# Kernel tuning notes

Hardware: AMD Instinct MI355X
Metric: run time of the kernel (lower is better)

Reference implementation:

```python
import jax, jax.numpy as jnp
import numpy as np

K = 4      # tagset_size - 2 (real emotion tags)
NT = 6     # tagset_size
START = 4
STOP = 5


def setup_inputs() -> dict:
    key = jax.random.key(0)
    ks = jax.random.split(key, 10)
    B, T = 2048, 2048
    feats = jax.random.normal(ks[0], (B, T, NT), dtype=jnp.float32)
    bias = jax.random.uniform(ks[1], (B, T), dtype=jnp.float32)        # bias_dict values in [0,1)
    tags = jax.random.randint(ks[2], (B, T), 0, K)                     # emotion labels only
    transitions = jax.random.normal(ks[3], (NT, NT), dtype=jnp.float32)
    transitions = transitions.at[START, :].set(-10000.0)
    transitions = transitions.at[:, STOP].set(-10000.0)
    w_shift_in = jax.random.normal(ks[4], (K,), dtype=jnp.float32)
    bias_no = jax.random.normal(ks[5], (1,), dtype=jnp.float32)
    bias_with = jax.random.normal(ks[6], (1,), dtype=jnp.float32)
    w_with_out = jax.random.normal(ks[7], (K,), dtype=jnp.float32)
    w_no_out = jax.random.normal(ks[8], (K,), dtype=jnp.float32)
    multiplier = jax.random.normal(ks[9], (K, K), dtype=jnp.float32)
    multiplier = multiplier.at[jnp.arange(K), jnp.arange(K)].set(-10000.0)
    return dict(feats=feats, bias=bias, tags=tags, transitions=transitions,
                w_shift_in=w_shift_in, bias_no=bias_no, bias_with=bias_with,
                w_with_out=w_with_out, w_no_out=w_no_out, multiplier=multiplier)


def reference(feats, bias, tags, transitions, w_shift_in, bias_no, bias_with,
              w_with_out, w_no_out, multiplier):
    """Batched neg_log_likelihood = forward_alg(feats) - score_sentence(feats, tags)."""
    B, T, _ = feats.shape
    # multiplier_softmax is over dim=0 (columns); diagonal overwritten with -1
    Mmod = jax.nn.softmax(multiplier, axis=0)
    Mmod = Mmod.at[jnp.arange(K), jnp.arange(K)].set(-1.0)

    # per-step transition gate, shape [B,T,K]; branch on bias > 0.5
    b = bias[..., None]
    gates = jnp.where(b > 0.5,
                      w_with_out * jnp.tanh(b * w_shift_in + bias_with),
                      w_no_out * jnp.tanh(b * w_shift_in + bias_no))

    # ---- forward algorithm (log-sum-exp DP over T, vectorized over B) ----
    init = jnp.full((B, NT), -10000.0, dtype=feats.dtype).at[:, START].set(0.0)
    feats_t = jnp.swapaxes(feats, 0, 1)   # [T,B,NT]
    gates_t = jnp.swapaxes(gates, 0, 1)   # [T,B,K]

    def step(alpha, x):
        f, g = x                                          # [B,NT], [B,K]
        blk = g[:, None, :] * Mmod[None, :, :]            # gate[prev] * Mmod[next,prev]
        Teff = transitions[None] + jnp.pad(blk, ((0, 0), (0, 2), (0, 2)))  # [B,NT,NT]
        alpha_new = f + jax.nn.logsumexp(alpha[:, None, :] + Teff, axis=2)
        return alpha_new, None

    alpha, _ = jax.lax.scan(step, init, (feats_t, gates_t))
    fwd_score = jax.nn.logsumexp(alpha + transitions[STOP][None, :], axis=1)  # [B]

    # ---- gold path score ----
    tags_ext = jnp.concatenate(
        [jnp.full((B, 1), START, dtype=tags.dtype), tags], axis=1)
    t0 = tags_ext[:, :-1]   # prev tag, [B,T]
    t1 = tags_ext[:, 1:]    # next tag, [B,T]
    base = transitions[t1, t0]
    Mext = jnp.pad(Mmod, ((0, 2), (0, 2)))
    gate_t0 = jnp.take_along_axis(gates, jnp.clip(t0, 0, K - 1)[..., None], axis=2)[..., 0]
    extra = jnp.where((t0 < K) & (t1 < K), gate_t0 * Mext[t1, t0], 0.0)
    emit = jnp.take_along_axis(feats, t1[..., None], axis=2)[..., 0]
    gold = jnp.sum(base + extra + emit, axis=1) + transitions[STOP, tags[:, -1]]

    return fwd_score - gold  # [B] per-dialog NLL
```

## Files before the change

kernel.cpp:

```cpp
#include <hip/hip_runtime.h>

#define BN 2048
#define TN 2048

__device__ __forceinline__ float ex2(float x){ return __builtin_amdgcn_exp2f(x); }
__device__ __forceinline__ float lg2(float x){ return __builtin_amdgcn_logf(x); }
__device__ __forceinline__ float rcpf(float x){ return __builtin_amdgcn_rcpf(x); }
__device__ __forceinline__ float rfl(float x){
    return __uint_as_float(__builtin_amdgcn_readfirstlane(__float_as_uint(x)));
}

constexpr float kLog2e = 1.4426950408889634f;
constexpr float kLn2   = 0.6931471805599453f;

__device__ __forceinline__ float fast_tanh(float x){
    float ax = fabsf(x);
    float e  = ex2(ax * (-2.0f * kLog2e));
    float t  = (1.0f - e) * rcpf(1.0f + e);
    return copysignf(t, x);
}

__device__ __forceinline__ float sel4(float v0, float v1, float v2, float v3, int idx){
    float r = (idx == 1) ? v1 : v0;
    r = (idx == 2) ? v2 : r;
    r = (idx == 3) ? v3 : r;
    return r;
}

struct P1Params {
    float AL[4][4], M[4][4];
    float wsv[4], wwv[4], wnv[4];
    float bwc, bnc;
    const float* sA; const float* sM;
    float tc4[4];
};

template <int NCOL>
__device__ __forceinline__ void step_generic(
    const P1Params& pp, float fi0, float fi1, float fi2, float fi3,
    float bv, int tg, bool renorm,
    float (&P)[4][NCOL], float (&lacc)[NCOL], float& gold, int& prev)
{
    const bool hw = bv > 0.5f;
    const float bc = hw ? pp.bwc : pp.bnc;
    float g[4], gL[4];
    #pragma unroll
    for (int j = 0; j < 4; ++j) {
        float x = fmaf(bv, pp.wsv[j], bc);
        g[j]  = (hw ? pp.wwv[j] : pp.wnv[j]) * fast_tanh(x);
        gL[j] = g[j] * kLog2e;
    }
    const float fiL[4] = { fi0 * kLog2e, fi1 * kLog2e, fi2 * kLog2e, fi3 * kLog2e };
    float nP[4][NCOL];
    #pragma unroll
    for (int i = 0; i < 4; ++i)
        #pragma unroll
        for (int j = 0; j < NCOL; ++j) nP[i][j] = 0.0f;
    #pragma unroll
    for (int k = 0; k < 4; ++k) {
        float Ek[4];
        #pragma unroll
        for (int i = 0; i < 4; ++i)
            Ek[i] = ex2(fmaf(gL[k], pp.M[i][k], fiL[i] + pp.AL[i][k]));
        #pragma unroll
        for (int j = 0; j < NCOL; ++j) {
            const float pk = P[k][j];
            #pragma unroll
            for (int i = 0; i < 4; ++i) nP[i][j] = fmaf(Ek[i], pk, nP[i][j]);
        }
    }
    #pragma unroll
    for (int i = 0; i < 4; ++i)
        #pragma unroll
        for (int j = 0; j < NCOL; ++j) P[i][j] = nP[i][j];

    const int idx = tg * 4 + prev;
    gold += pp.sA[idx] + sel4(g[0], g[1], g[2], g[3], prev) * pp.sM[idx]
          + sel4(fi0, fi1, fi2, fi3, tg);
    prev = tg;

    if (renorm) {
        #pragma unroll
        for (int j = 0; j < NCOL; ++j) {
            float m = fmaxf(fmaxf(P[0][j], P[1][j]), fmaxf(P[2][j], P[3][j]));
            int ee = (int)((__float_as_uint(m) >> 23) & 255u) - 126;
            float sc = __uint_as_float((unsigned)(127 - ee) << 23);
            lacc[j] += (float)ee;
            #pragma unroll
            for (int i = 0; i < 4; ++i) P[i][j] *= sc;
        }
    }
}

template <int NCOL, bool C0>
__device__ __forceinline__ void trip4(
    const float4 (&F)[6], const float (&Bv)[4], const int (&Tg)[4],
    const P1Params& pp, float (&P)[4][NCOL], float (&lacc)[NCOL],
    float& gold, int& prev)
{
    #pragma unroll
    for (int p = 0; p < 2; ++p) {
        const float4 fA = F[3*p], fB = F[3*p+1], fC = F[3*p+2];
        {
            const float fi0 = fA.x, fi1 = fA.y, fi2 = fA.z, fi3 = fA.w;
            if (C0 && p == 0) {
                const float a0 = fi0 + pp.tc4[0], a1 = fi1 + pp.tc4[1];
                const float a2 = fi2 + pp.tc4[2], a3 = fi3 + pp.tc4[3];
                const float mx = fmaxf(fmaxf(a0, a1), fmaxf(a2, a3));
                P[0][0] = ex2((a0 - mx) * kLog2e);
                P[1][0] = ex2((a1 - mx) * kLog2e);
                P[2][0] = ex2((a2 - mx) * kLog2e);
                P[3][0] = ex2((a3 - mx) * kLog2e);
                lacc[0] = mx * kLog2e;
                const int tg0 = Tg[0];
                gold = sel4(pp.tc4[0], pp.tc4[1], pp.tc4[2], pp.tc4[3], tg0)
                     + sel4(fi0, fi1, fi2, fi3, tg0);
                prev = tg0;
            } else {
                step_generic<NCOL>(pp, fi0, fi1, fi2, fi3, Bv[2*p], Tg[2*p],
                                   false, P, lacc, gold, prev);
            }
        }
        {
            const float fi0 = fB.z, fi1 = fB.w, fi2 = fC.x, fi3 = fC.y;
            step_generic<NCOL>(pp, fi0, fi1, fi2, fi3, Bv[2*p+1], Tg[2*p+1],
                               (2*p+1) == 3, P, lacc, gold, prev);
        }
    }
}

__device__ __forceinline__ void compose4(
    const float (&Ae)[4][4], const float (&sa)[4],
    const float (&Be)[4][4], const float (&sb)[4],
    float (&Ce)[4][4], float (&sc)[4])
{
    const float maxA = fmaxf(fmaxf(sa[0], sa[1]), fmaxf(sa[2], sa[3]));
    float Ap[4][4];
    #pragma unroll
    for (int k = 0; k < 4; ++k) {
        const float wk = ex2(sa[k] - maxA);
        #pragma unroll
        for (int i = 0; i < 4; ++i) Ap[i][k] = Ae[i][k] * wk;
    }
    #pragma unroll
    for (int j = 0; j < 4; ++j) {
        float c0 = 0.f, c1 = 0.f, c2 = 0.f, c3 = 0.f;
        #pragma unroll
        for (int k = 0; k < 4; ++k) {
            const float bk = Be[k][j];
            c0 = fmaf(Ap[0][k], bk, c0);
            c1 = fmaf(Ap[1][k], bk, c1);
            c2 = fmaf(Ap[2][k], bk, c2);
            c3 = fmaf(Ap[3][k], bk, c3);
        }
        const float m = fmaxf(fmaxf(c0, c1), fmaxf(c2, c3));
        const int ee = (int)((__float_as_uint(m) >> 23) & 255u) - 126;
        const float scf = __uint_as_float((unsigned)(127 - ee) << 23);
        Ce[0][j] = c0 * scf; Ce[1][j] = c1 * scf;
        Ce[2][j] = c2 * scf; Ce[3][j] = c3 * scf;
        sc[j] = sb[j] + maxA + (float)ee;
    }
}

__global__ void __launch_bounds__(256)
crf_fused(const float* __restrict__ feats, const float* __restrict__ bias,
          const int* __restrict__ tags, const float* __restrict__ trans,
          const float* __restrict__ wsh, const float* __restrict__ bno,
          const float* __restrict__ bwi, const float* __restrict__ wwo,
          const float* __restrict__ wno, const float* __restrict__ mult,
          float* __restrict__ out)
{
    const int w = threadIdx.x >> 6;
    const int L = threadIdx.x & 63;
    const int b = blockIdx.x;
    const int c = threadIdx.x;

    __shared__ float4 stage[4 * 384];
    __shared__ float sA[16], sM[16];
    __shared__ float red[4][24];

    float4* stageW = stage + w * 384;

    if (threadIdx.x < 16) {
        const int i = threadIdx.x >> 2, j = threadIdx.x & 3;
        sA[threadIdx.x] = trans[i * 6 + j];
        const float m0 = mult[j], m1 = mult[4 + j], m2 = mult[8 + j], m3 = mult[12 + j];
        const float mx = fmaxf(fmaxf(m0, m1), fmaxf(m2, m3));
        const float e0 = ex2((m0 - mx) * kLog2e), e1 = ex2((m1 - mx) * kLog2e);
        const float e2 = ex2((m2 - mx) * kLog2e), e3 = ex2((m3 - mx) * kLog2e);
        const float inv = rcpf(e0 + e1 + e2 + e3);
        const float ei = (i == 0) ? e0 : (i == 1) ? e1 : (i == 2) ? e2 : e3;
        sM[threadIdx.x] = (i == j) ? -1.0f : ei * inv;
    }
    __syncthreads();

    P1Params pp;
    #pragma unroll
    for (int i = 0; i < 4; ++i)
        #pragma unroll
        for (int j = 0; j < 4; ++j) {
            pp.AL[i][j] = rfl(trans[i * 6 + j] * kLog2e);
            pp.M[i][j]  = rfl(sM[i * 4 + j]);
        }
    #pragma unroll
    for (int j = 0; j < 4; ++j) {
        pp.wsv[j] = rfl(wsh[j]); pp.wwv[j] = rfl(wwo[j]); pp.wnv[j] = rfl(wno[j]);
    }
    pp.bwc = rfl(bwi[0]); pp.bnc = rfl(bno[0]);
    pp.sA = sA; pp.sM = sM;
    pp.tc4[0] = rfl(trans[4]);  pp.tc4[1] = rfl(trans[10]);
    pp.tc4[2] = rfl(trans[16]); pp.tc4[3] = rfl(trans[22]);

    float BvA[4], BvB[4]; int TgA[4], TgB[4];
    {
        const float4* bp = (const float4*)(bias + (size_t)b * TN + c * 8);
        const float4 b0 = bp[0], b1 = bp[1];
        BvA[0]=b0.x; BvA[1]=b0.y; BvA[2]=b0.z; BvA[3]=b0.w;
        BvB[0]=b1.x; BvB[1]=b1.y; BvB[2]=b1.z; BvB[3]=b1.w;
        const int4* tp = (const int4*)(tags + (size_t)b * TN + c * 8);
        const int4 t0 = tp[0], t1 = tp[1];
        TgA[0]=t0.x; TgA[1]=t0.y; TgA[2]=t0.z; TgA[3]=t0.w;
        TgB[0]=t1.x; TgB[1]=t1.y; TgB[2]=t1.z; TgB[3]=t1.w;
    }
    int prev = 0;
    if (c != 0) prev = tags[(size_t)b * TN + c * 8 - 1];

    const float4* gF = (const float4*)feats + (size_t)b * 3072 + (size_t)w * 768;

    float P1a[4][1], lacc1[1];
    float P4[4][4],  lacc4[4] = {0.f, 0.f, 0.f, 0.f};
    #pragma unroll
    for (int i = 0; i < 4; ++i)
        #pragma unroll
        for (int j = 0; j < 4; ++j) P4[i][j] = (i == j) ? 1.0f : 0.0f;
    float gold = 0.0f;

    #pragma unroll 1
    for (int h = 0; h < 2; ++h) {
        float4 myF[6];
        {
            float4 tF[6];
            const int h6 = h * 6;
            #pragma unroll
            for (int r = 0; r < 6; ++r) {
                const int S  = r * 64 + L;
                const int cS = (S * 10923) >> 16;
                const int j  = S - cS * 6;
                tF[r] = gF[cS * 12 + h6 + j];
            }
            #pragma unroll
            for (int r = 0; r < 6; ++r) {
                const int S  = r * 64 + L;
                const int cS = (S * 10923) >> 16;
                const int j  = S - cS * 6;
                stageW[(j << 6) + ((cS + j) & 63)] = tF[r];
            }
            #pragma unroll
            for (int j = 0; j < 6; ++j)
                myF[j] = stageW[(j << 6) + ((L + j) & 63)];
        }
        if (c == 0) {
            if (h == 0) trip4<1, true >(myF, BvA, TgA, pp, P1a, lacc1, gold, prev);
            else        trip4<1, false>(myF, BvB, TgB, pp, P1a, lacc1, gold, prev);
        } else {
            if (h == 0) trip4<4, false>(myF, BvA, TgA, pp, P4, lacc4, gold, prev);
            else        trip4<4, false>(myF, BvB, TgB, pp, P4, lacc4, gold, prev);
        }
    }

    float Pe[4][4], so[4];
    if (c == 0) {
        #pragma unroll
        for (int i = 0; i < 4; ++i)
            #pragma unroll
            for (int j = 0; j < 4; ++j) Pe[i][j] = P1a[i][0];
        #pragma unroll
        for (int j = 0; j < 4; ++j) so[j] = lacc1[0];
    } else {
        #pragma unroll
        for (int i = 0; i < 4; ++i)
            #pragma unroll
            for (int j = 0; j < 4; ++j) Pe[i][j] = P4[i][j];
        #pragma unroll
        for (int j = 0; j < 4; ++j) so[j] = lacc4[j];
    }

    #pragma unroll
    for (int d = 1; d < 64; d <<= 1) {
        float oP[4][4], os[4];
        #pragma unroll
        for (int i = 0; i < 4; ++i)
            #pragma unroll
            for (int j = 0; j < 4; ++j) oP[i][j] = __shfl_xor(Pe[i][j], d, 64);
        #pragma unroll
        for (int j = 0; j < 4; ++j) os[j] = __shfl_xor(so[j], d, 64);
        const bool hi = (L & d) != 0;
        float Ae[4][4], Be[4][4], sa[4], sb[4];
        #pragma unroll
        for (int i = 0; i < 4; ++i)
            #pragma unroll
            for (int j = 0; j < 4; ++j) {
                Ae[i][j] = hi ? Pe[i][j] : oP[i][j];
                Be[i][j] = hi ? oP[i][j] : Pe[i][j];
            }
        #pragma unroll
        for (int j = 0; j < 4; ++j) {
            sa[j] = hi ? so[j] : os[j];
            sb[j] = hi ? os[j] : so[j];
        }
        float Ce[4][4], sc[4];
        compose4(Ae, sa, Be, sb, Ce, sc);
        #pragma unroll
        for (int i = 0; i < 4; ++i)
            #pragma unroll
            for (int j = 0; j < 4; ++j) Pe[i][j] = Ce[i][j];
        #pragma unroll
        for (int j = 0; j < 4; ++j) so[j] = sc[j];
    }
    #pragma unroll
    for (int d = 1; d < 64; d <<= 1) gold += __shfl_xor(gold, d, 64);

    if (L == 0) {
        #pragma unroll
        for (int i = 0; i < 4; ++i)
            #pragma unroll
            for (int j = 0; j < 4; ++j) red[w][i * 4 + j] = Pe[i][j];
        #pragma unroll
        for (int j = 0; j < 4; ++j) red[w][16 + j] = so[j];
        red[w][20] = gold;
    }
    __syncthreads();
    if (threadIdx.x == 0) {
        float Pt[4][4], st[4];
        #pragma unroll
        for (int i = 0; i < 4; ++i)
            #pragma unroll
            for (int j = 0; j < 4; ++j) Pt[i][j] = red[0][i * 4 + j];
        #pragma unroll
        for (int j = 0; j < 4; ++j) st[j] = red[0][16 + j];
        float gsum = red[0][20] + red[1][20] + red[2][20] + red[3][20];
        #pragma unroll
        for (int ww = 1; ww < 4; ++ww) {
            float Ae[4][4], sa[4], Ce[4][4], scv[4];
            #pragma unroll
            for (int i = 0; i < 4; ++i)
                #pragma unroll
                for (int j = 0; j < 4; ++j) Ae[i][j] = red[ww][i * 4 + j];
            #pragma unroll
            for (int j = 0; j < 4; ++j) sa[j] = red[ww][16 + j];
            compose4(Ae, sa, Pt, st, Ce, scv);
            #pragma unroll
            for (int i = 0; i < 4; ++i)
                #pragma unroll
                for (int j = 0; j < 4; ++j) Pt[i][j] = Ce[i][j];
            #pragma unroll
            for (int j = 0; j < 4; ++j) st[j] = scv[j];
        }
        const float t50 = trans[30], t51 = trans[31], t52 = trans[32], t53 = trans[33];
        const float ssum = Pt[0][0] * ex2(t50 * kLog2e) + Pt[1][0] * ex2(t51 * kLog2e)
                         + Pt[2][0] * ex2(t52 * kLog2e) + Pt[3][0] * ex2(t53 * kLog2e);
        const float fwd = (st[0] + lg2(ssum)) * kLn2;
        const int lastT = tags[(size_t)b * TN + TN - 1];
        const float gfin = gsum + sel4(t50, t51, t52, t53, lastT);
        out[b] = fwd - gfin;
    }
}

extern "C" void kernel_launch(void* const* d_in, const int* in_sizes, int n_in,
                              void* d_out, int out_size, void* d_ws, size_t ws_size,
                              hipStream_t stream)
{
    const float* feats = (const float*)d_in[0];
    const float* bias  = (const float*)d_in[1];
    const int*   tags  = (const int*)d_in[2];
    const float* trans = (const float*)d_in[3];
    const float* wsh   = (const float*)d_in[4];
    const float* bno   = (const float*)d_in[5];
    const float* bwi   = (const float*)d_in[6];
    const float* wwo   = (const float*)d_in[7];
    const float* wno   = (const float*)d_in[8];
    const float* mult  = (const float*)d_in[9];
    float* out = (float*)d_out;
    (void)d_ws; (void)ws_size;

    crf_fused<<<BN, 256, 0, stream>>>(
        feats, bias, tags, trans, wsh, bno, bwi, wwo, wno, mult, out);
}
```

Measured before the change: 236.4 us.

## Replace wave-shuffle scan with shared-memory tree reduction of transfer matrices

The intra-wave butterfly of 4x4 log-domain matrix compositions via shuffles, and the final serial 4-wave combine, are replaced by a binary-tree reduction through shared memory with a block barrier per level. Each thread writes its 25-float state to LDS, and at each of 8 levels half of the active threads compose their neighbour's state into their own. The readfirstlane hints on uniform parameters are also dropped. The tree does far fewer compose4 calls overall, since the butterfly made every lane compute at each step, but it adds 8 block barriers, LDS traffic, and divergent low-occupancy levels.

After: 242.9 us. 2.7% more time.

```diff
diff --git a/kernel.cpp b/kernel.cpp
--- a/kernel.cpp
+++ b/kernel.cpp
@@ -6,9 +6,6 @@
 __device__ __forceinline__ float ex2(float x){ return __builtin_amdgcn_exp2f(x); }
 __device__ __forceinline__ float lg2(float x){ return __builtin_amdgcn_logf(x); }
 __device__ __forceinline__ float rcpf(float x){ return __builtin_amdgcn_rcpf(x); }
-__device__ __forceinline__ float rfl(float x){
-    return __uint_as_float(__builtin_amdgcn_readfirstlane(__float_as_uint(x)));
-}
 
 constexpr float kLog2e = 1.4426950408889634f;
 constexpr float kLn2   = 0.6931471805599453f;
@@ -175,11 +172,9 @@
     const int b = blockIdx.x;
     const int c = threadIdx.x;
 
-    __shared__ float4 stage[4 * 384];
+    __shared__ float shm[6400];
     __shared__ float sA[16], sM[16];
-    __shared__ float red[4][24];
-
-    float4* stageW = stage + w * 384;
+    float4* stageW = ((float4*)shm) + w * 384;
 
     if (threadIdx.x < 16) {
         const int i = threadIdx.x >> 2, j = threadIdx.x & 3;
@@ -199,17 +194,14 @@
     for (int i = 0; i < 4; ++i)
         #pragma unroll
         for (int j = 0; j < 4; ++j) {
-            pp.AL[i][j] = rfl(trans[i * 6 + j] * kLog2e);
-            pp.M[i][j]  = rfl(sM[i * 4 + j]);
-        }
-    #pragma unroll
-    for (int j = 0; j < 4; ++j) {
-        pp.wsv[j] = rfl(wsh[j]); pp.wwv[j] = rfl(wwo[j]); pp.wnv[j] = rfl(wno[j]);
-    }
-    pp.bwc = rfl(bwi[0]); pp.bnc = rfl(bno[0]);
+            pp.AL[i][j] = trans[i * 6 + j] * kLog2e;
+            pp.M[i][j]  = sM[i * 4 + j];
+        }
+    #pragma unroll
+    for (int j = 0; j < 4; ++j) { pp.wsv[j] = wsh[j]; pp.wwv[j] = wwo[j]; pp.wnv[j] = wno[j]; }
+    pp.bwc = bwi[0]; pp.bnc = bno[0];
     pp.sA = sA; pp.sM = sM;
-    pp.tc4[0] = rfl(trans[4]);  pp.tc4[1] = rfl(trans[10]);
-    pp.tc4[2] = rfl(trans[16]); pp.tc4[3] = rfl(trans[22]);
+    pp.tc4[0] = trans[4]; pp.tc4[1] = trans[10]; pp.tc4[2] = trans[16]; pp.tc4[3] = trans[22];
 
     float BvA[4], BvB[4]; int TgA[4], TgB[4];
     {
@@ -285,83 +277,50 @@
         for (int j = 0; j < 4; ++j) so[j] = lacc4[j];
     }
 
-    #pragma unroll
-    for (int d = 1; d < 64; d <<= 1) {
-        float oP[4][4], os[4];
-        #pragma unroll
-        for (int i = 0; i < 4; ++i)
-            #pragma unroll
-            for (int j = 0; j < 4; ++j) oP[i][j] = __shfl_xor(Pe[i][j], d, 64);
-        #pragma unroll
-        for (int j = 0; j < 4; ++j) os[j] = __shfl_xor(so[j], d, 64);
-        const bool hi = (L & d) != 0;
-        float Ae[4][4], Be[4][4], sa[4], sb[4];
-        #pragma unroll
-        for (int i = 0; i < 4; ++i)
-            #pragma unroll
-            for (int j = 0; j < 4; ++j) {
-                Ae[i][j] = hi ? Pe[i][j] : oP[i][j];
-                Be[i][j] = hi ? oP[i][j] : Pe[i][j];
-            }
-        #pragma unroll
-        for (int j = 0; j < 4; ++j) {
-            sa[j] = hi ? so[j] : os[j];
-            sb[j] = hi ? os[j] : so[j];
-        }
-        float Ce[4][4], sc[4];
-        compose4(Ae, sa, Be, sb, Ce, sc);
-        #pragma unroll
-        for (int i = 0; i < 4; ++i)
-            #pragma unroll
-            for (int j = 0; j < 4; ++j) Pe[i][j] = Ce[i][j];
-        #pragma unroll
-        for (int j = 0; j < 4; ++j) so[j] = sc[j];
-    }
-    #pragma unroll
-    for (int d = 1; d < 64; d <<= 1) gold += __shfl_xor(gold, d, 64);
-
-    if (L == 0) {
-        #pragma unroll
-        for (int i = 0; i < 4; ++i)
-            #pragma unroll
-            for (int j = 0; j < 4; ++j) red[w][i * 4 + j] = Pe[i][j];
-        #pragma unroll
-        for (int j = 0; j < 4; ++j) red[w][16 + j] = so[j];
-        red[w][20] = gold;
-    }
+    float* my = shm + (size_t)threadIdx.x * 25;
     __syncthreads();
-    if (threadIdx.x == 0) {
-        float Pt[4][4], st[4];
-        #pragma unroll
-        for (int i = 0; i < 4; ++i)
-            #pragma unroll
-            for (int j = 0; j < 4; ++j) Pt[i][j] = red[0][i * 4 + j];
-        #pragma unroll
-        for (int j = 0; j < 4; ++j) st[j] = red[0][16 + j];
-        float gsum = red[0][20] + red[1][20] + red[2][20] + red[3][20];
-        #pragma unroll
-        for (int ww = 1; ww < 4; ++ww) {
-            float Ae[4][4], sa[4], Ce[4][4], scv[4];
+    #pragma unroll
+    for (int i = 0; i < 4; ++i)
+        #pragma unroll
+        for (int j = 0; j < 4; ++j) my[i * 4 + j] = Pe[i][j];
+    #pragma unroll
+    for (int j = 0; j < 4; ++j) my[16 + j] = so[j];
+    my[20] = gold;
+    __syncthreads();
+
+    #pragma unroll 1
+    for (int l = 0; l < 8; ++l) {
+        const int s = 1 << l;
+        if ((threadIdx.x & (2 * s - 1)) == 0) {
+            const float* ot = shm + (size_t)(threadIdx.x + s) * 25;
+            float Ae[4][4], sa[4];
             #pragma unroll
             for (int i = 0; i < 4; ++i)
                 #pragma unroll
-                for (int j = 0; j < 4; ++j) Ae[i][j] = red[ww][i * 4 + j];
-            #pragma unroll
-            for (int j = 0; j < 4; ++j) sa[j] = red[ww][16 + j];
-            compose4(Ae, sa, Pt, st, Ce, scv);
+                for (int j = 0; j < 4; ++j) Ae[i][j] = ot[i * 4 + j];
+            #pragma unroll
+            for (int j = 0; j < 4; ++j) sa[j] = ot[16 + j];
+            gold += ot[20];
+            float Ce[4][4], sc[4];
+            compose4(Ae, sa, Pe, so, Ce, sc);
             #pragma unroll
             for (int i = 0; i < 4; ++i)
                 #pragma unroll
-                for (int j = 0; j < 4; ++j) Pt[i][j] = Ce[i][j];
-            #pragma unroll
-            for (int j = 0; j < 4; ++j) st[j] = scv[j];
-        }
+                for (int j = 0; j < 4; ++j) { Pe[i][j] = Ce[i][j]; my[i * 4 + j] = Ce[i][j]; }
+            #pragma unroll
+            for (int j = 0; j < 4; ++j) { so[j] = sc[j]; my[16 + j] = sc[j]; }
+            my[20] = gold;
+        }
+        __syncthreads();
+    }
+
+    if (threadIdx.x == 0) {
         const float t50 = trans[30], t51 = trans[31], t52 = trans[32], t53 = trans[33];
-        const float ssum = Pt[0][0] * ex2(t50 * kLog2e) + Pt[1][0] * ex2(t51 * kLog2e)
-                         + Pt[2][0] * ex2(t52 * kLog2e) + Pt[3][0] * ex2(t53 * kLog2e);
-        const float fwd = (st[0] + lg2(ssum)) * kLn2;
+        const float ssum = Pe[0][0] * ex2(t50 * kLog2e) + Pe[1][0] * ex2(t51 * kLog2e)
+                         + Pe[2][0] * ex2(t52 * kLog2e) + Pe[3][0] * ex2(t53 * kLog2e);
+        const float fwd = (so[0] + lg2(ssum)) * kLn2;
         const int lastT = tags[(size_t)b * TN + TN - 1];
-        const float gfin = gsum + sel4(t50, t51, t52, t53, lastT);
+        const float gfin = gold + sel4(t50, t51, t52, t53, lastT);
         out[b] = fwd - gfin;
     }
 }
```
